# Optimization experiments

Hardware: AMD Instinct MI355X
Metric: run time of the kernel (lower is better)

## Reference

```python
import jax, jax.numpy as jnp
import numpy as np

NS = 16384  # number of samples
N = 2048    # number of sites


def setup_inputs() -> dict:
    key = jax.random.key(0)
    kx, kk = jax.random.split(key)
    x = jax.random.normal(kx, (NS, N), dtype=jnp.float32)
    kernel = 0.01 * jax.random.normal(kk, (N * (N - 1) // 2,), dtype=jnp.float32)
    return {"x": x, "kernel": kernel, "n": 4}


def reference(x, kernel, n):
    # Build strictly lower-triangular W from the kernel vector (sorted, unique indices)
    Nloc = x.shape[-1]
    il = jnp.tril_indices(Nloc, k=-1)
    W = jnp.zeros((Nloc, Nloc), dtype=kernel.dtype).at[il].set(
        kernel, unique_indices=True, indices_are_sorted=True)
    # z_nj = sum_i x_ni W_ji  ==  x @ W.T
    z = x @ W.T
    # each step: z_nk = sum_j z_nj W_kj x_nj  ==  (z * x) @ W.T
    z = jax.lax.fori_loop(0, n - 2, lambda i, zz: (zz * x) @ W.T, z)
    # logpsi_n = sum_l z_nl x_nl
    return jnp.sum(z * x, axis=-1)
```

## Files before the change

kernel.cpp:

```cpp
#include <hip/hip_runtime.h>
#include <stdint.h>

#define NSAMP 16384
#define NSITE 2048
#define BM 128
#define BN 256
#define BK 64

typedef _Float16 f16x8 __attribute__((ext_vector_type(8)));
typedef float f32x16 __attribute__((ext_vector_type(16)));

__device__ __forceinline__ unsigned short f2h(float f) {
  _Float16 h = (_Float16)f;
  return __builtin_bit_cast(unsigned short, h);
}
__device__ __forceinline__ float h2f(unsigned short u) {
  return (float)__builtin_bit_cast(_Float16, u);
}

__device__ __forceinline__ void gload_lds16(const void* g, void* l) {
  __builtin_amdgcn_global_load_lds(
      (const __attribute__((address_space(1))) void*)g,
      (__attribute__((address_space(3))) void*)l, 16, 0, 0);
}


__global__ void build_w_kernel(const float* __restrict__ kern,
                               unsigned short* __restrict__ Wp) {
  const int idx = blockIdx.x * blockDim.x + threadIdx.x;
  const int lane = idx & 63;
  const int kb = (idx >> 6) & 127;
  const int rbG = idx >> 13;
  const int j = rbG * 32 + (lane & 31);
  const int i0 = kb * 16 + (lane >> 5) * 8;
  const long long tri = (long long)j * (j - 1) / 2;
  unsigned short v[8];
#pragma unroll
  for (int e = 0; e < 8; ++e) {
    const int i = i0 + e;
    float f = (i < j) ? kern[tri + i] : 0.0f;
    v[e] = f2h(f);
  }
  ushort4* dst = (ushort4*)(Wp + (size_t)idx * 8);
  dst[0] = make_ushort4(v[0], v[1], v[2], v[3]);
  dst[1] = make_ushort4(v[4], v[5], v[6], v[7]);
}

__global__ void build_x_kernel(const float* __restrict__ x,
                               unsigned short* __restrict__ Xp,
                               unsigned short* __restrict__ Xrow) {
  const int idx = blockIdx.x * blockDim.x + threadIdx.x;
  const int row = idx >> 8;
  const int c8 = idx & 255;
  const float4 v0 = ((const float4*)x)[(size_t)idx * 2];
  const float4 v1 = ((const float4*)x)[(size_t)idx * 2 + 1];
  const ushort4 h0 = make_ushort4(f2h(v0.x), f2h(v0.y), f2h(v0.z), f2h(v0.w));
  const ushort4 h1 = make_ushort4(f2h(v1.x), f2h(v1.y), f2h(v1.z), f2h(v1.w));
  ushort4* dr = (ushort4*)(Xrow + (size_t)idx * 8);
  dr[0] = h0;
  dr[1] = h1;
  const int rbG = row >> 5, kb = c8 >> 1;
  const int lane = (c8 & 1) * 32 + (row & 31);
  ushort4* dp = (ushort4*)(Xp + (((size_t)rbG * 128 + kb) * 64 + lane) * 8);
  dp[0] = h0;
  dp[1] = h1;
}

template <int EPI>
__global__ __launch_bounds__(512, 4) void gemm_pass(
    const unsigned short* __restrict__ Ap, const unsigned short* __restrict__ Wp,
    const unsigned short* __restrict__ Xrow, unsigned short* __restrict__ Pp,
    float* __restrict__ out) {
  __shared__ unsigned short lds[24576];

  const int bid = blockIdx.x;
  const int g = bid >> 7;
  const int nt = (g & 1) ? (g >> 1) : (7 - (g >> 1));
  const int mt = bid & 127;
  const int m0 = mt * BM, n0 = nt * BN;

  const int tid = threadIdx.x, lane = tid & 63, wid = tid >> 6;
  const int wm = wid >> 2;
  const int wn = wid & 3;
  const int l32 = lane & 31, hi2 = lane >> 5;
  const int nkt = 4 * (nt + 1);

  f32x16 acc[2][2] = {};

  const int rbG0 = m0 >> 5, cbG0 = n0 >> 5;
  const unsigned short* srcA[2];
  int dstA[2];
#pragma unroll
  for (int r = 0; r < 2; ++r) {
    const int fA = r * 8 + wid;
    srcA[r] = Ap + ((size_t)(rbG0 + (fA >> 2)) * 128 + (fA & 3)) * 512 + lane * 8;
    dstA[r] = fA * 1024 + lane * 16;
  }
  const unsigned short* srcW[4];
  int dstW[4];
#pragma unroll
  for (int r = 0; r < 4; ++r) {
    const int fW = r * 8 + wid;
    srcW[r] = Wp + ((size_t)(cbG0 + (fW >> 2)) * 128 + (fW & 3)) * 512 + lane * 8;
    dstW[r] = 16384 + fW * 1024 + lane * 16;
  }

  for (int kt = 0; kt < nkt; ++kt) {
    const size_t ko = (size_t)kt * 2048;
#pragma unroll
    for (int r = 0; r < 2; ++r) gload_lds16(srcA[r] + ko, (char*)lds + dstA[r]);
#pragma unroll
    for (int r = 0; r < 4; ++r) gload_lds16(srcW[r] + ko, (char*)lds + dstW[r]);
    __syncthreads();
#pragma unroll
    for (int kbl = 0; kbl < 4; ++kbl) {
      f16x8 a0 = *(const f16x8*)((char*)lds + ((wm * 2 + 0) * 4 + kbl) * 1024 + lane * 16);
      f16x8 a1 = *(const f16x8*)((char*)lds + ((wm * 2 + 1) * 4 + kbl) * 1024 + lane * 16);
      f16x8 b0 = *(const f16x8*)((char*)lds + 16384 + ((wn * 2 + 0) * 4 + kbl) * 1024 + lane * 16);
      f16x8 b1 = *(const f16x8*)((char*)lds + 16384 + ((wn * 2 + 1) * 4 + kbl) * 1024 + lane * 16);
      acc[0][0] = __builtin_amdgcn_mfma_f32_32x32x16_f16(a0, b0, acc[0][0], 0, 0, 0);
      acc[0][1] = __builtin_amdgcn_mfma_f32_32x32x16_f16(a0, b1, acc[0][1], 0, 0, 0);
      acc[1][0] = __builtin_amdgcn_mfma_f32_32x32x16_f16(a1, b0, acc[1][0], 0, 0, 0);
      acc[1][1] = __builtin_amdgcn_mfma_f32_32x32x16_f16(a1, b1, acc[1][1], 0, 0, 0);
    }
    __syncthreads();
  }

  const int ebase = wid * 4096;
  if (EPI == 0) {
#pragma unroll
    for (int mb = 0; mb < 2; ++mb) {
      const int growb = m0 + wm * 64 + mb * 32;
#pragma unroll
      for (int nb = 0; nb < 2; ++nb)
#pragma unroll
        for (int r = 0; r < 16; ++r) {
          const int row = (r & 3) + 8 * (r >> 2) + 4 * hi2;
          const int col = nb * 32 + l32;
          const unsigned short xv =
              Xrow[(size_t)(growb + row) * NSITE + n0 + wn * 64 + col];
          const unsigned short pv = f2h(acc[mb][nb][r] * h2f(xv));
          const int cbyte = (col * 2) ^ ((row & 7) << 4);
          *((unsigned short*)((char*)lds + ebase + row * 128 + cbyte)) = pv;
        }
      __syncthreads();
      const int rbG = growb >> 5;
#pragma unroll
      for (int kbl = 0; kbl < 4; ++kbl) {
        const int cbyteR = (kbl * 32 + hi2 * 16) ^ ((l32 & 7) << 4);
        f16x8 fr = *(const f16x8*)((char*)lds + ebase + l32 * 128 + cbyteR);
        const int kbG = ((n0 + wn * 64) >> 4) + kbl;
        *(f16x8*)(Pp + (((size_t)rbG * 128 + kbG) * 64 + lane) * 8) = fr;
      }
      __syncthreads();
    }
  } else {
#pragma unroll
    for (int mb = 0; mb < 2; ++mb) {
      const int growb = m0 + wm * 64 + mb * 32;
#pragma unroll
      for (int r = 0; r < 16; ++r) {
        const int row = (r & 3) + 8 * (r >> 2) + 4 * hi2;
        const int grow = growb + row;
        const size_t xb = (size_t)grow * NSITE + n0 + wn * 64 + l32;
        float s = acc[mb][0][r] * h2f(Xrow[xb]) + acc[mb][1][r] * h2f(Xrow[xb + 32]);
        s += __shfl_xor(s, 1);
        s += __shfl_xor(s, 2);
        s += __shfl_xor(s, 4);
        s += __shfl_xor(s, 8);
        s += __shfl_xor(s, 16);
        if (l32 == 0) atomicAdd(&out[grow], s);
      }
    }
  }
}

extern "C" void kernel_launch(void* const* d_in, const int* in_sizes, int n_in,
                              void* d_out, int out_size, void* d_ws, size_t ws_size,
                              hipStream_t stream) {
  const float* x = (const float*)d_in[0];
  const float* kern = (const float*)d_in[1];
  float* out = (float*)d_out;

  unsigned short* Wp   = (unsigned short*)d_ws;
  unsigned short* Xp   = Wp + (size_t)NSITE * NSITE;
  unsigned short* Xrow = Xp + (size_t)NSAMP * NSITE;
  unsigned short* P1   = Xrow + (size_t)NSAMP * NSITE;
  unsigned short* P2   = P1 + (size_t)NSAMP * NSITE;

  hipMemsetAsync(d_out, 0, (size_t)NSAMP * sizeof(float), stream);
  build_w_kernel<<<(NSITE * NSITE / 8) / 256, 256, 0, stream>>>(kern, Wp);
  build_x_kernel<<<(NSAMP * NSITE / 8) / 256, 256, 0, stream>>>(x, Xp, Xrow);

  gemm_pass<0><<<1024, 512, 0, stream>>>(Xp, Wp, Xrow, P1, nullptr);
  gemm_pass<0><<<1024, 512, 0, stream>>>(P1, Wp, Xrow, P2, nullptr);
  gemm_pass<1><<<1024, 512, 0, stream>>>(P2, Wp, Xrow, nullptr, out);
}
```

Before: 419.9 us.

## Double-buffer LDS tiles with a K-step of 32 in the GEMM passes

Halves the K tile from 64 to 32 and splits the shared LDS array into two buffers. Each iteration issues the asynchronous global-to-LDS loads for the next K tile before running the MFMAs on the current tile, so memory fetch can overlap with compute. This replaces the load-sync-compute-sync pattern. In exchange there are twice as many loop iterations and barriers, and each barrier covers less MFMA work.

After: 409.5 us. 2.5% less time.

```diff
diff --git a/kernel.cpp b/kernel.cpp
--- a/kernel.cpp
+++ b/kernel.cpp
@@ -5,7 +5,7 @@
 #define NSITE 2048
 #define BM 128
 #define BN 256
-#define BK 64
+#define BK 32
 
 typedef _Float16 f16x8 __attribute__((ext_vector_type(8)));
 typedef float f32x16 __attribute__((ext_vector_type(16)));
@@ -83,41 +83,40 @@
   const int wm = wid >> 2;
   const int wn = wid & 3;
   const int l32 = lane & 31, hi2 = lane >> 5;
-  const int nkt = 4 * (nt + 1);
+  const int nkt = 8 * (nt + 1);
 
   f32x16 acc[2][2] = {};
 
   const int rbG0 = m0 >> 5, cbG0 = n0 >> 5;
-  const unsigned short* srcA[2];
-  int dstA[2];
+  const int fA = tid >> 6;
+  const unsigned short* srcA =
+      Ap + ((size_t)(rbG0 + (fA >> 1)) * 128 + (fA & 1)) * 512 + lane * 8;
+  const unsigned short* srcW[2];
 #pragma unroll
   for (int r = 0; r < 2; ++r) {
-    const int fA = r * 8 + wid;
-    srcA[r] = Ap + ((size_t)(rbG0 + (fA >> 2)) * 128 + (fA & 3)) * 512 + lane * 8;
-    dstA[r] = fA * 1024 + lane * 16;
-  }
-  const unsigned short* srcW[4];
-  int dstW[4];
-#pragma unroll
-  for (int r = 0; r < 4; ++r) {
-    const int fW = r * 8 + wid;
-    srcW[r] = Wp + ((size_t)(cbG0 + (fW >> 2)) * 128 + (fW & 3)) * 512 + lane * 8;
-    dstW[r] = 16384 + fW * 1024 + lane * 16;
+    const int fW = r * 8 + (tid >> 6);
+    srcW[r] = Wp + ((size_t)(cbG0 + (fW >> 1)) * 128 + (fW & 1)) * 512 + lane * 8;
   }
 
+  auto STAGE = [&](int kt, int bufbase) {
+    const size_t ko = (size_t)kt * 1024;
+    gload_lds16(srcA + ko, (char*)lds + bufbase + tid * 16);
+    gload_lds16(srcW[0] + ko, (char*)lds + bufbase + 8192 + tid * 16);
+    gload_lds16(srcW[1] + ko, (char*)lds + bufbase + 16384 + tid * 16);
+  };
+
+  STAGE(0, 0);
+  __syncthreads();
+
   for (int kt = 0; kt < nkt; ++kt) {
-    const size_t ko = (size_t)kt * 2048;
+    const int cur = (kt & 1) * 24576;
+    if (kt + 1 < nkt) STAGE(kt + 1, cur ^ 24576);
 #pragma unroll
-    for (int r = 0; r < 2; ++r) gload_lds16(srcA[r] + ko, (char*)lds + dstA[r]);
-#pragma unroll
-    for (int r = 0; r < 4; ++r) gload_lds16(srcW[r] + ko, (char*)lds + dstW[r]);
-    __syncthreads();
-#pragma unroll
-    for (int kbl = 0; kbl < 4; ++kbl) {
-      f16x8 a0 = *(const f16x8*)((char*)lds + ((wm * 2 + 0) * 4 + kbl) * 1024 + lane * 16);
-      f16x8 a1 = *(const f16x8*)((char*)lds + ((wm * 2 + 1) * 4 + kbl) * 1024 + lane * 16);
-      f16x8 b0 = *(const f16x8*)((char*)lds + 16384 + ((wn * 2 + 0) * 4 + kbl) * 1024 + lane * 16);
-      f16x8 b1 = *(const f16x8*)((char*)lds + 16384 + ((wn * 2 + 1) * 4 + kbl) * 1024 + lane * 16);
+    for (int kbl = 0; kbl < 2; ++kbl) {
+      f16x8 a0 = *(const f16x8*)((char*)lds + cur + (((wm * 2 + 0) * 2 + kbl)) * 1024 + lane * 16);
+      f16x8 a1 = *(const f16x8*)((char*)lds + cur + (((wm * 2 + 1) * 2 + kbl)) * 1024 + lane * 16);
+      f16x8 b0 = *(const f16x8*)((char*)lds + cur + 8192 + (((wn * 2 + 0) * 2 + kbl)) * 1024 + lane * 16);
+      f16x8 b1 = *(const f16x8*)((char*)lds + cur + 8192 + (((wn * 2 + 1) * 2 + kbl)) * 1024 + lane * 16);
       acc[0][0] = __builtin_amdgcn_mfma_f32_32x32x16_f16(a0, b0, acc[0][0], 0, 0, 0);
       acc[0][1] = __builtin_amdgcn_mfma_f32_32x32x16_f16(a0, b1, acc[0][1], 0, 0, 0);
       acc[1][0] = __builtin_amdgcn_mfma_f32_32x32x16_f16(a1, b0, acc[1][0], 0, 0, 0);
```
